# Kernel optimization log

Hardware: AMD Instinct MI355X
Metric: run time of the kernel (lower is better)

The kernel has to match this reference:

```python
import jax, jax.numpy as jnp
import numpy as np

UP = 2          # upsample factor used by upfirdn2d.upsample2d default
FILTER = [1, 2, 1]


def _make_fir_kernel():
    # CreateLowpassKernel: convolve([1,2,1],[1,1]) -> [1,3,3,1]; outer product; normalize.
    k1 = np.convolve(np.asarray(FILTER, np.float32), [1.0, 1.0]).reshape(1, -1)
    k = k1.T @ k1
    k = k / k.sum()
    # upsample2d applies gain = up**2
    return jnp.asarray(k * (UP ** 2), dtype=jnp.float32)  # [4,4]


def setup_inputs() -> dict:
    key = jax.random.key(0)
    kx, kw = jax.random.split(key)
    B, Cin, Cout, H, W = 16, 512, 512, 64, 64
    x = jax.random.normal(kx, (B, Cin, H, W), dtype=jnp.float32)
    fir_kernel = _make_fir_kernel()
    # MSR init for 1x1 conv: std = 1/sqrt(in_ch * k*k) = 1/sqrt(Cin)
    w = jax.random.normal(kw, (Cout, Cin, 1, 1), dtype=jnp.float32) / np.sqrt(Cin)
    b = jnp.zeros((Cout,), dtype=jnp.float32)
    return {"x": x, "fir_kernel": fir_kernel, "w": w, "b": b}


def _upsample2d(x, fir_kernel):
    # upfirdn2d: zero-insert by UP, pad ((fw+UP-1)//2, (fw-UP)//2) = (2,1), convolve with flipped FIR.
    C = x.shape[1]
    fw = fir_kernel.shape[-1]
    k = fir_kernel[::-1, ::-1]                       # flip -> true convolution
    dw = jnp.broadcast_to(k, (C, 1, fw, fw))         # depthwise kernel [C,1,4,4]
    pad = ((fw + UP - 1) // 2, (fw - UP) // 2)       # (2, 1)
    return jax.lax.conv_general_dilated(
        x, dw,
        window_strides=(1, 1),
        padding=(pad, pad),
        lhs_dilation=(UP, UP),                       # zero-insertion upsample
        dimension_numbers=("NCHW", "OIHW", "NCHW"),
        feature_group_count=C,
    )


def reference(x, fir_kernel, w, b):
    y = _upsample2d(x, fir_kernel)                   # [B,C,2H,2W]
    # Convolution.forward nan/inf guard (no-op for finite inputs)
    y = jnp.nan_to_num(y, nan=0.0, posinf=1.0, neginf=-1.0)
    # 1x1 conv projection + bias
    out = jnp.einsum("bchw,oc->bohw", y, w[:, :, 0, 0]) + b[None, :, None, None]
    return out
```

## Files before the change

### kernel.cpp

```cpp
#include <hip/hip_runtime.h>


#define B_   16
#define CIN  512
#define COUT 512
#define S_   4096
#define HO   127
#define WO   127

typedef unsigned int  u32;
typedef unsigned short u16;
typedef __attribute__((ext_vector_type(8))) short  bf16x8;
typedef __attribute__((ext_vector_type(8))) u16    u16x8;
typedef __attribute__((ext_vector_type(4))) float  f32x4;

static __device__ __forceinline__ u16 f2bf(float f) {
  u32 u = __float_as_uint(f);
  u += 0x7FFFu + ((u >> 16) & 1u);
  return (u16)(u >> 16);
}
static __device__ __forceinline__ float bf2f(u16 h) {
  return __uint_as_float(((u32)h) << 16);
}

#if defined(__has_builtin)
#if __has_builtin(__builtin_amdgcn_global_load_lds)
#define HAS_GLOAD 1
#endif
#endif
#ifndef HAS_GLOAD
#define HAS_GLOAD 0
#endif

#if HAS_GLOAD
static __device__ __forceinline__ void gload16(const char* g, char* l) {
  __builtin_amdgcn_global_load_lds(
      (const __attribute__((address_space(1))) unsigned int*)g,
      (__attribute__((address_space(3))) unsigned int*)l, 16, 0, 0);
}
#endif


__global__ __launch_bounds__(256) void conv_w_kernel(
    const float* __restrict__ w, u16* __restrict__ wt) {
  int g = blockIdx.x * 256 + threadIdx.x;
  int t_idx = g >> 9;
  int u = g & 511;
  int to = t_idx >> 4, tk = t_idx & 15;
  int r = u & 127, kg = u >> 7;
  int o = to * 128 + r;
  int c = tk * 32 + kg * 8;
  const float4* src = reinterpret_cast<const float4*>(w + (size_t)o * CIN + c);
  float4 lo = src[0], hi = src[1];
  u16x8 pk;
  pk[0] = f2bf(lo.x); pk[1] = f2bf(lo.y); pk[2] = f2bf(lo.z); pk[3] = f2bf(lo.w);
  pk[4] = f2bf(hi.x); pk[5] = f2bf(hi.y); pk[6] = f2bf(hi.z); pk[7] = f2bf(hi.w);
  *reinterpret_cast<u16x8*>(wt + (size_t)g * 8) = pk;
}

__global__ __launch_bounds__(256) void conv_x_kernel(
    const float* __restrict__ x, u16* __restrict__ xt) {
  int ts = blockIdx.x, tk = blockIdx.y, b = blockIdx.z;
  int t = threadIdx.x;
  __shared__ float lf[32 * 128];
  const float* src = x + ((size_t)(b * CIN + tk * 32)) * S_ + ts * 128;
#pragma unroll
  for (int i = 0; i < 4; ++i) {
    int q = i * 256 + t;
    int c = q >> 5, sq = q & 31;
    *reinterpret_cast<float4*>(&lf[c * 128 + sq * 4]) =
        *reinterpret_cast<const float4*>(src + (size_t)c * S_ + sq * 4);
  }
  __syncthreads();
  size_t tile_base = (((size_t)(b * 32 + ts)) * 16 + tk) * 512;
#pragma unroll
  for (int i = 0; i < 2; ++i) {
    int u = i * 256 + t;
    int kg = u >> 7, r = u & 127;
    u16x8 pk;
#pragma unroll
    for (int e = 0; e < 8; ++e) pk[e] = f2bf(lf[(kg * 8 + e) * 128 + r]);
    *reinterpret_cast<u16x8*>(xt + (tile_base + u) * 8) = pk;
  }
}

__global__ __launch_bounds__(256) void gemm_kernel(
    const u16* __restrict__ wt, const u16* __restrict__ xt,
    u16* __restrict__ z) {
  int nt = blockIdx.x, mt = blockIdx.y, b = blockIdx.z;
  int t = threadIdx.x;
  __shared__ short lds[8192];
  char* lA = (char*)&lds[0];
  char* lB = lA + 8192;

  int lane = t & 63, wid = t >> 6;
  int wr = wid >> 1, wc = wid & 1;
  int lr = lane & 15, kg = lane >> 4;

  f32x4 acc[4][4];
#pragma unroll
  for (int m = 0; m < 4; ++m)
#pragma unroll
    for (int n = 0; n < 4; ++n) acc[m][n] = f32x4{0.f, 0.f, 0.f, 0.f};

  const char* gA = (const char*)wt + (size_t)(mt * 16) * 8192;
  const char* gB = (const char*)xt + ((size_t)(b * 32 + nt)) * 16 * 8192;

  int abyte[4], bbyte[4];
#pragma unroll
  for (int m = 0; m < 4; ++m) abyte[m] = (kg * 128 + wr * 64 + m * 16 + lr) * 16;
#pragma unroll
  for (int n = 0; n < 4; ++n) bbyte[n] = (kg * 128 + wc * 64 + n * 16 + lr) * 16;

  for (int ks = 0; ks < 16; ++ks) {
    const char* pA = gA + (size_t)ks * 8192;
    const char* pB = gB + (size_t)ks * 8192;
#if HAS_GLOAD
    __syncthreads();
    gload16(pA + t * 16, lA + t * 16);
    gload16(pA + 4096 + t * 16, lA + 4096 + t * 16);
    gload16(pB + t * 16, lB + t * 16);
    gload16(pB + 4096 + t * 16, lB + 4096 + t * 16);
    __syncthreads();
#else
    u16x8 va0 = *reinterpret_cast<const u16x8*>(pA + t * 16);
    u16x8 va1 = *reinterpret_cast<const u16x8*>(pA + 4096 + t * 16);
    u16x8 vb0 = *reinterpret_cast<const u16x8*>(pB + t * 16);
    u16x8 vb1 = *reinterpret_cast<const u16x8*>(pB + 4096 + t * 16);
    __syncthreads();
    *reinterpret_cast<u16x8*>(lA + t * 16) = va0;
    *reinterpret_cast<u16x8*>(lA + 4096 + t * 16) = va1;
    *reinterpret_cast<u16x8*>(lB + t * 16) = vb0;
    *reinterpret_cast<u16x8*>(lB + 4096 + t * 16) = vb1;
    __syncthreads();
#endif
    bf16x8 av[4], bv[4];
#pragma unroll
    for (int m = 0; m < 4; ++m)
      av[m] = *reinterpret_cast<const bf16x8*>(lA + abyte[m]);
#pragma unroll
    for (int n = 0; n < 4; ++n)
      bv[n] = *reinterpret_cast<const bf16x8*>(lB + bbyte[n]);
#pragma unroll
    for (int m = 0; m < 4; ++m)
#pragma unroll
      for (int n = 0; n < 4; ++n)
        acc[m][n] = __builtin_amdgcn_mfma_f32_16x16x32_bf16(
            av[m], bv[n], acc[m][n], 0, 0, 0);
  }

  int o_b = mt * 128 + wr * 64 + kg * 4;
  int s_b = nt * 128 + wc * 64 + lr;
#pragma unroll
  for (int m = 0; m < 4; ++m)
#pragma unroll
    for (int n = 0; n < 4; ++n) {
      f32x4 v = acc[m][n];
      size_t base = ((size_t)(b * COUT + o_b + m * 16)) * S_ + (s_b + n * 16);
#pragma unroll
      for (int r = 0; r < 4; ++r) z[base + (size_t)r * S_] = f2bf(v[r]);
    }
}

__global__ __launch_bounds__(256) void upsample_kernel(
    const u16* __restrict__ z, const float* __restrict__ bias,
    float* __restrict__ out) {
  const u32 TOT = (u32)B_ * COUT * HO;
  u32 H = gridDim.x * 8u;
  u32 hid = blockIdx.x * 8u + (threadIdx.x >> 5);
  int l = threadIdx.x & 31;
  int lp = (l == 0) ? 0 : l - 1;
  int ln = (l == 31) ? 31 : l + 1;
  float tA0 = (l == 0) ? 0.f : 1.f;
  bool full = (l < 31);

  for (u32 rg = hid; rg < TOT; rg += H) {
    u32 img = rg / 127u;
    u32 r = rg - img * 127u;
    const u32* zi = reinterpret_cast<const u32*>(z) + ((size_t)img << 11);
    float bv = bias[img & 511u];

    u32 m = (r + 1) >> 1;
    int a = (int)m - 1;
    float wa = (r & 1) ? 3.f : 1.f;
    float wb = (r & 1) ? 1.f : 3.f;
    if (a < 0) { a = 0; wa = 0.f; }

    const u32* rA = zi + a * 32;
    const u32* rB = zi + (int)m * 32;
    u32 Pa = rA[lp], Ca = rA[l], Na = rA[ln];
    u32 Pb = rB[lp], Cb = rB[l], Nb = rB[ln];

    float a0 = bf2f((u16)Ca), a1 = bf2f((u16)(Ca >> 16));
    float aP = bf2f((u16)(Pa >> 16)), aN = bf2f((u16)Na);
    float gA0 = fmaf(3.f, a0, tA0 * aP);
    float gA1 = fmaf(3.f, a0, a1);
    float gA2 = fmaf(3.f, a1, a0);
    float gA3 = fmaf(3.f, a1, aN);

    float b0 = bf2f((u16)Cb), b1 = bf2f((u16)(Cb >> 16));
    float bP = bf2f((u16)(Pb >> 16)), bN = bf2f((u16)Nb);
    float gB0 = fmaf(3.f, b0, tA0 * bP);
    float gB1 = fmaf(3.f, b0, b1);
    float gB2 = fmaf(3.f, b1, b0);
    float gB3 = fmaf(3.f, b1, bN);

    float v0 = fmaf(fmaf(wa, gA0, wb * gB0), 0.0625f, bv);
    float v1 = fmaf(fmaf(wa, gA1, wb * gB1), 0.0625f, bv);
    float v2 = fmaf(fmaf(wa, gA2, wb * gB2), 0.0625f, bv);
    float v3 = fmaf(fmaf(wa, gA3, wb * gB3), 0.0625f, bv);

    float* po = out + (size_t)rg * WO + 4 * l;
    if (full) {
      float vv[4] = {v0, v1, v2, v3};
      __builtin_memcpy(po, vv, 16);
    } else {
      po[0] = v0; po[1] = v1; po[2] = v2;
    }
  }
}

__global__ __launch_bounds__(256) void fallback_kernel(
    const float* __restrict__ x, const float* __restrict__ w,
    const float* __restrict__ bias, float* __restrict__ out) {
  u32 idx = blockIdx.x * 256u + threadIdx.x;
  const u32 total = (u32)B_ * COUT * HO * WO;
  if (idx >= total) return;
  u32 j = idx % WO;
  u32 r1 = idx / WO;
  u32 i = r1 % HO;
  u32 bo = r1 / HO;
  int o = (int)(bo & 511u);
  int b = (int)(bo >> 9);
  int m = (int)(i >> 1), n = (int)(j >> 1);
  int ie = !(i & 1), je = !(j & 1);
  int rA = ie ? m - 1 : m;
  int cA = je ? n - 1 : n;
  float w_r0 = ie ? 1.f : 3.f, w_r1 = ie ? 3.f : 1.f;
  float w_c0 = je ? 1.f : 3.f, w_c1 = je ? 3.f : 1.f;
  const float* xb = x + (size_t)b * CIN * S_;
  float acc = 0.f;
  for (int cc = 0; cc < CIN; ++cc) {
    const float* xc = xb + (size_t)cc * S_;
    float y = 0.f;
    if (rA >= 0) {
      if (cA >= 0) y += w_r0 * w_c0 * xc[rA * 64 + cA];
      y += w_r0 * w_c1 * xc[rA * 64 + cA + 1];
    }
    if (cA >= 0) y += w_r1 * w_c0 * xc[(rA + 1) * 64 + cA];
    y += w_r1 * w_c1 * xc[(rA + 1) * 64 + cA + 1];
    acc += y * w[(size_t)o * CIN + cc];
  }
  out[idx] = acc * 0.0625f + bias[o];
}

extern "C" void kernel_launch(void* const* d_in, const int* in_sizes, int n_in,
                              void* d_out, int out_size, void* d_ws,
                              size_t ws_size, hipStream_t stream) {
  const float* x = (const float*)d_in[0];
  const float* w = (const float*)d_in[2];
  const float* bias = (const float*)d_in[3];
  float* out = (float*)d_out;

  const size_t xt_bytes = (size_t)B_ * S_ * CIN * 2;
  const size_t wt_off = xt_bytes;
  const size_t wt_bytes = (size_t)COUT * CIN * 2;
  const size_t z_off = wt_off + ((wt_bytes + 255) & ~(size_t)255);
  const size_t need = z_off + (size_t)B_ * COUT * S_ * 2;
  const size_t total_out = (size_t)B_ * COUT * HO * WO;
  const u32 nblk_out = (u32)((total_out + 255) / 256);

  if (ws_size >= need) {
    u16* xt = (u16*)d_ws;
    u16* wt = (u16*)((char*)d_ws + wt_off);
    u16* zz = (u16*)((char*)d_ws + z_off);
    conv_w_kernel<<<128, 256, 0, stream>>>(w, wt);
    conv_x_kernel<<<dim3(32, 16, B_), 256, 0, stream>>>(x, xt);
    gemm_kernel<<<dim3(32, 4, B_), 256, 0, stream>>>(wt, xt, zz);
    upsample_kernel<<<2048, 256, 0, stream>>>(zz, bias, out);
  } else {
    fallback_kernel<<<nblk_out, 256, 0, stream>>>(x, w, bias, out);
  }
}
```

Measured before the change: 280.7 us.

## Fuse upsample epilogue into GEMM via LDS tile, handle tile-boundary rows separately

The GEMM kernel now stages its bf16 output tile in shared memory and directly computes the FIR-upsampled output rows that depend only on the two input rows inside the tile. A separate boundary kernel computes the remaining output rows, which straddle tile boundaries, from the bf16 z buffer that is still written to global memory. The aim is to avoid re-reading most of z in a separate pass. The cost is about 33 KB of extra LDS per block, which may lower occupancy, plus a strided per-lane store pattern in the epilogue.

```diff
diff --git a/kernel.cpp b/kernel.cpp
--- a/kernel.cpp
+++ b/kernel.cpp
@@ -12,6 +12,7 @@
 typedef unsigned short u16;
 typedef __attribute__((ext_vector_type(8))) short  bf16x8;
 typedef __attribute__((ext_vector_type(8))) u16    u16x8;
+typedef __attribute__((ext_vector_type(4))) u16    u16x4;
 typedef __attribute__((ext_vector_type(4))) float  f32x4;
 
 static __device__ __forceinline__ u16 f2bf(float f) {
@@ -84,12 +85,15 @@
   }
 }
 
-__global__ __launch_bounds__(256) void gemm_kernel(
+#define ZP 132
+__global__ __launch_bounds__(256) void gemm_fused_kernel(
     const u16* __restrict__ wt, const u16* __restrict__ xt,
-    u16* __restrict__ z) {
+    const float* __restrict__ bias, u16* __restrict__ z,
+    float* __restrict__ out) {
   int nt = blockIdx.x, mt = blockIdx.y, b = blockIdx.z;
   int t = threadIdx.x;
   __shared__ short lds[8192];
+  __shared__ u16 zl[128 * ZP];
   char* lA = (char*)&lds[0];
   char* lB = lA + 8192;
 
@@ -156,16 +160,72 @@
 #pragma unroll
     for (int n = 0; n < 4; ++n) {
       f32x4 v = acc[m][n];
+      u16 h[4];
+#pragma unroll
+      for (int r = 0; r < 4; ++r) h[r] = f2bf(v[r]);
       size_t base = ((size_t)(b * COUT + o_b + m * 16)) * S_ + (s_b + n * 16);
 #pragma unroll
-      for (int r = 0; r < 4; ++r) z[base + (size_t)r * S_] = f2bf(v[r]);
+      for (int r = 0; r < 4; ++r) z[base + (size_t)r * S_] = h[r];
+      int s_loc = wc * 64 + n * 16 + lr;
+      int o_loc = wr * 64 + m * 16 + kg * 4;
+      u16x4 pk; pk[0] = h[0]; pk[1] = h[1]; pk[2] = h[2]; pk[3] = h[3];
+      *reinterpret_cast<u16x4*>(&zl[s_loc * ZP + o_loc]) = pk;
     }
-}
-
-__global__ __launch_bounds__(256) void upsample_kernel(
+  __syncthreads();
+
+  {
+    int c = t & 15, og = t >> 4;
+    int n0 = 4 * c - 1;
+    int i00 = (c == 0) ? 0 : n0;
+#pragma unroll
+    for (int i = 0; i < 8; ++i) {
+      int o_l = og + 16 * i;
+      int o_glob = mt * 128 + o_l;
+      float bv = bias[o_glob];
+      float a6[6], d6[6];
+      a6[0] = bf2f(zl[i00 * ZP + o_l]);
+      d6[0] = bf2f(zl[(64 + i00) * ZP + o_l]);
+#pragma unroll
+      for (int k = 1; k < 6; ++k) {
+        a6[k] = bf2f(zl[(n0 + k) * ZP + o_l]);
+        d6[k] = bf2f(zl[(64 + n0 + k) * ZP + o_l]);
+      }
+      float v1[8], v2[8], v0[8];
+#pragma unroll
+      for (int e = 0; e < 8; ++e) {
+        int li = (e == 0) ? 0 : (1 + ((e - 1) >> 1));
+        float tA = (e & 1) ? 3.f : 1.f;
+        float tB = (e & 1) ? 1.f : 3.f;
+        if (c == 0 && e == 0) tA = 0.f;
+        float g0 = tA * a6[li] + tB * a6[li + 1];
+        float g1 = tA * d6[li] + tB * d6[li + 1];
+        v1[e] = fmaf(fmaf(3.f, g0, g1), 0.0625f, bv);
+        v2[e] = fmaf(fmaf(3.f, g1, g0), 0.0625f, bv);
+        v0[e] = fmaf(3.f * g0, 0.0625f, bv);
+      }
+      size_t ob = ((size_t)(b * COUT + o_glob)) * (size_t)(HO * WO) + 8 * c;
+      float* p1 = out + ob + (size_t)(4 * nt + 1) * WO;
+      float* p2 = p1 + WO;
+      if (c < 15) {
+        __builtin_memcpy(p1, v1, 32);
+        __builtin_memcpy(p2, v2, 32);
+        if (nt == 0) __builtin_memcpy(out + ob, v0, 32);
+      } else {
+        __builtin_memcpy(p1, v1, 16); __builtin_memcpy(p1 + 4, &v1[4], 8); p1[6] = v1[6];
+        __builtin_memcpy(p2, v2, 16); __builtin_memcpy(p2 + 4, &v2[4], 8); p2[6] = v2[6];
+        if (nt == 0) {
+          float* p0 = out + ob;
+          __builtin_memcpy(p0, v0, 16); __builtin_memcpy(p0 + 4, &v0[4], 8); p0[6] = v0[6];
+        }
+      }
+    }
+  }
+}
+
+__global__ __launch_bounds__(256) void boundary_kernel(
     const u16* __restrict__ z, const float* __restrict__ bias,
     float* __restrict__ out) {
-  const u32 TOT = (u32)B_ * COUT * HO;
+  const u32 TOT = (u32)B_ * COUT * 62u;
   u32 H = gridDim.x * 8u;
   u32 hid = blockIdx.x * 8u + (threadIdx.x >> 5);
   int l = threadIdx.x & 31;
@@ -174,20 +234,20 @@
   float tA0 = (l == 0) ? 0.f : 1.f;
   bool full = (l < 31);
 
-  for (u32 rg = hid; rg < TOT; rg += H) {
-    u32 img = rg / 127u;
-    u32 r = rg - img * 127u;
+  for (u32 q = hid; q < TOT; q += H) {
+    u32 img = q / 62u;
+    u32 rid = q - img * 62u;
+    u32 a = rid >> 1;
+    u32 r = 4u * a + 3u + (rid & 1u);
+    u32 m = 2u * a + 2u;
+    float wa = (rid & 1u) ? 1.f : 3.f;
+    float wb = (rid & 1u) ? 3.f : 1.f;
+
     const u32* zi = reinterpret_cast<const u32*>(z) + ((size_t)img << 11);
     float bv = bias[img & 511u];
 
-    u32 m = (r + 1) >> 1;
-    int a = (int)m - 1;
-    float wa = (r & 1) ? 3.f : 1.f;
-    float wb = (r & 1) ? 1.f : 3.f;
-    if (a < 0) { a = 0; wa = 0.f; }
-
-    const u32* rA = zi + a * 32;
-    const u32* rB = zi + (int)m * 32;
+    const u32* rA = zi + (m - 1) * 32;
+    const u32* rB = zi + m * 32;
     u32 Pa = rA[lp], Ca = rA[l], Na = rA[ln];
     u32 Pb = rB[lp], Cb = rB[l], Nb = rB[ln];
 
@@ -210,7 +270,7 @@
     float v2 = fmaf(fmaf(wa, gA2, wb * gB2), 0.0625f, bv);
     float v3 = fmaf(fmaf(wa, gA3, wb * gB3), 0.0625f, bv);
 
-    float* po = out + (size_t)rg * WO + 4 * l;
+    float* po = out + ((size_t)img * HO + r) * WO + 4 * l;
     if (full) {
       float vv[4] = {v0, v1, v2, v3};
       __builtin_memcpy(po, vv, 16);
@@ -276,8 +336,8 @@
     u16* zz = (u16*)((char*)d_ws + z_off);
     conv_w_kernel<<<128, 256, 0, stream>>>(w, wt);
     conv_x_kernel<<<dim3(32, 16, B_), 256, 0, stream>>>(x, xt);
-    gemm_kernel<<<dim3(32, 4, B_), 256, 0, stream>>>(wt, xt, zz);
-    upsample_kernel<<<2048, 256, 0, stream>>>(zz, bias, out);
+    gemm_fused_kernel<<<dim3(32, 4, B_), 256, 0, stream>>>(wt, xt, bias, zz, out);
+    boundary_kernel<<<2048, 256, 0, stream>>>(zz, bias, out);
   } else {
     fallback_kernel<<<nblk_out, 256, 0, stream>>>(x, w, bias, out);
   }
```

Result: slower. 350.4 us (+24.8%).
